# Performance work log

Measured on AMD Instinct MI355X. Metric: run time of the kernel, lower is better.

## Reference

```python
import jax, jax.numpy as jnp
import numpy as np

B, S, D = 4, 2048, 1024
H, HK = 16, 4          # num_heads, num_heads_kv
HD = D // H            # head_dim = 64
G = H // HK            # kv groups = 4


def setup_inputs() -> dict:
    key = jax.random.key(0)
    ks = jax.random.split(key, 7)
    s = 0.02
    return {
        "query": jax.random.normal(ks[0], (B, S, D), jnp.float32),
        "key":   jax.random.normal(ks[1], (B, S, D), jnp.float32),
        "value": jax.random.normal(ks[2], (B, S, D), jnp.float32),
        # weights stored (in, out); equivalent to torch Linear y = x @ W.T
        "Wq": jax.random.normal(ks[3], (D, H * HD), jnp.float32) * s,
        "Wk": jax.random.normal(ks[4], (D, HK * HD), jnp.float32) * s,
        "Wv": jax.random.normal(ks[5], (D, HK * HD), jnp.float32) * s,
        "Wo": jax.random.normal(ks[6], (H * HD, D), jnp.float32) * s,
    }


def reference(query, key, value, Wq, Wk, Wv, Wo):
    b, qlen, _ = query.shape
    kvlen = key.shape[1]
    # projections
    q = (query @ Wq).reshape(b, qlen, H, HD)        # [b,q,H,hd]
    k = (key @ Wk).reshape(b, kvlen, HK, HD)        # [b,s,HK,hd]
    v = (value @ Wv).reshape(b, kvlen, HK, HD)      # [b,s,HK,hd]
    # GQA: q head h attends kv head h//G (repeat_interleave semantics)
    qg = q.reshape(b, qlen, HK, G, HD)              # head = kv*G + group
    scale = 1.0 / jnp.sqrt(jnp.asarray(HD, q.dtype))
    # scores [b,HK,G,q,s] -- broadcast kv heads, no materialized repeat
    scores = jnp.einsum('bqkgd,bskd->bkgqs', qg, k) * scale
    attn = jax.nn.softmax(scores, axis=-1)
    out = jnp.einsum('bkgqs,bskd->bqkgd', attn, v)  # [b,q,HK,G,hd]
    out = out.reshape(b, qlen, H * HD)
    return out @ Wo
```

## Files before the change

kernel.cpp:

```cpp
#include <hip/hip_runtime.h>


typedef unsigned short u16;
typedef unsigned int   u32;
typedef __bf16 bf16x4 __attribute__((ext_vector_type(4)));
typedef __bf16 bf16x8 __attribute__((ext_vector_type(8)));
typedef float  f32x4  __attribute__((ext_vector_type(4)));

#define MFMA(a,b,c) __builtin_amdgcn_mfma_f32_16x16x32_bf16((a),(b),(c),0,0,0)

#define GLDS(g, l) __builtin_amdgcn_global_load_lds(                          \
    (const __attribute__((address_space(1))) void*)(g),                       \
    (__attribute__((address_space(3))) void*)(l), 16, 0, 0)

#if __has_builtin(__builtin_amdgcn_exp2f)
#define EXP2(x) __builtin_amdgcn_exp2f(x)
#else
#define EXP2(x) exp2f(x)
#endif

__device__ __forceinline__ u16 f2bf(float f){
    u32 u = __builtin_bit_cast(u32, f);
    u += 0x7fffu + ((u >> 16) & 1u);
    return (u16)(u >> 16);
}
__device__ __forceinline__ u32 pk2(float a, float b){
#if __has_builtin(__builtin_amdgcn_cvt_pk_bf16_f32)
    auto r = __builtin_amdgcn_cvt_pk_bf16_f32(a, b);
    return __builtin_bit_cast(u32, r);
#else
    return (u32)f2bf(a) | ((u32)f2bf(b) << 16);
#endif
}
__device__ __forceinline__ bf16x8 ldfrag(const u16* p){
    return *(const bf16x8*)p;
}
__device__ __forceinline__ bf16x8 ld2x64(const u16* p){
    bf16x4 lo = *(const bf16x4*)p;
    bf16x4 hi = *(const bf16x4*)(p + 4);
    bf16x8 r;
    r[0]=lo[0]; r[1]=lo[1]; r[2]=lo[2]; r[3]=lo[3];
    r[4]=hi[0]; r[5]=hi[1]; r[6]=hi[2]; r[7]=hi[3];
    return r;
}

__global__ __launch_bounds__(256) void prep(const float* __restrict__ q,
                                            const float* __restrict__ k,
                                            const float* __restrict__ v,
                                            const float* __restrict__ Wq,
                                            const float* __restrict__ Wk,
                                            const float* __restrict__ Wv,
                                            const float* __restrict__ Wo,
                                            u16* Qc, u16* Kc, u16* Vc,
                                            u16* WqT, u16* WkT, u16* WvT, u16* WoT){
    const int tid = threadIdx.x, bid = blockIdx.x;
    if (bid < 2560){
        __shared__ float T[32][33];
        const float* W; u16* WT; int N, i;
        if (bid < 1024)      { W = Wq; WT = WqT; N = 1024; i = bid; }
        else if (bid < 1280) { W = Wk; WT = WkT; N =  256; i = bid - 1024; }
        else if (bid < 1536) { W = Wv; WT = WvT; N =  256; i = bid - 1280; }
        else                 { W = Wo; WT = WoT; N = 1024; i = bid - 1536; }
        int kt = (i & 31) * 32, nt = (i >> 5) * 32;
        int r = tid >> 3, c = tid & 7;
        float4 vv = *(const float4*)(W + (size_t)(kt + r) * N + nt + c * 4);
        T[r][c*4+0] = vv.x; T[r][c*4+1] = vv.y; T[r][c*4+2] = vv.z; T[r][c*4+3] = vv.w;
        __syncthreads();
        u32 lo = pk2(T[c*4+0][r], T[c*4+1][r]);
        u32 hi = pk2(T[c*4+2][r], T[c*4+3][r]);
        *(uint2*)(WT + (size_t)(nt + r) * 1024 + kt + c * 4) = make_uint2(lo, hi);
    } else {
        int i = bid - 2560;
        const float* src = (i < 512) ? q : (i < 1024 ? k : v);
        u16*         dst = (i < 512) ? Qc : (i < 1024 ? Kc : Vc);
        size_t off = (size_t)(i & 511) * 16384;
        const float* s = src + off;
        u16* d = dst + off;
        #pragma unroll
        for (int p = 0; p < 16; ++p){
            int idx = (p * 256 + tid) * 4;
            float4 vv = *(const float4*)(s + idx);
            *(uint2*)(d + idx) = make_uint2(pk2(vv.x, vv.y), pk2(vv.z, vv.w));
        }
    }
}

template<int EPI>
__device__ __forceinline__ void gemm_body(const u16* __restrict__ A,
                                          const u16* __restrict__ Bt,
                                          void* __restrict__ Cp,
                                          int N, int K, int m0, int n0,
                                          u16* As, u16* Bs, float oscale){
    const int tid  = threadIdx.x;
    const int wave = tid >> 6, lane = tid & 63;
    const int quad = lane >> 4, l15 = lane & 15;
    const int wm = wave >> 1, wn = wave & 1;
    const int srow = lane >> 3;
    const int scol = ((lane & 7) ^ srow) * 8;
    const int swz  = l15 & 7;

    f32x4 acc[4][4];
    #pragma unroll
    for (int i = 0; i < 4; ++i)
        #pragma unroll
        for (int j = 0; j < 4; ++j) acc[i][j] = (f32x4){0.f, 0.f, 0.f, 0.f};

    const int nkt = K >> 6;
    for (int kt = 0; kt < nkt; ++kt){
        __syncthreads();
        {
            const u16* ga = A + (size_t)(m0 + wave*32 + srow) * K + kt*64 + scol;
            u16* la = As + (wave*32) * 64;
            #pragma unroll
            for (int p = 0; p < 4; ++p)
                GLDS(ga + (size_t)(p*8) * K, la + p*8*64);
            const u16* gb = Bt + (size_t)(n0 + wave*32 + srow) * K + kt*64 + scol;
            u16* lb = Bs + (wave*32) * 64;
            #pragma unroll
            for (int p = 0; p < 4; ++p)
                GLDS(gb + (size_t)(p*8) * K, lb + p*8*64);
        }
        __syncthreads();
        #pragma unroll
        for (int ks = 0; ks < 2; ++ks){
            bf16x8 af[4], bfr[4];
            #pragma unroll
            for (int mt = 0; mt < 4; ++mt)
                af[mt] = ldfrag(&As[(wm*64 + mt*16 + l15) * 64 +
                                    (((ks*4 + quad) ^ swz) * 8)]);
            #pragma unroll
            for (int nt = 0; nt < 4; ++nt)
                bfr[nt] = ldfrag(&Bs[(wn*64 + nt*16 + l15) * 64 +
                                     (((ks*4 + quad) ^ swz) * 8)]);
            #pragma unroll
            for (int mt = 0; mt < 4; ++mt)
                #pragma unroll
                for (int nt = 0; nt < 4; ++nt){
                    if constexpr (EPI == 1)
                        acc[mt][nt] = MFMA(af[mt], bfr[nt], acc[mt][nt]);
                    else
                        acc[mt][nt] = MFMA(bfr[nt], af[mt], acc[mt][nt]);
                }
        }
    }
    #pragma unroll
    for (int mt = 0; mt < 4; ++mt){
        #pragma unroll
        for (int nt = 0; nt < 4; ++nt){
            if constexpr (EPI == 1){
                int rowb = m0 + wm*64 + mt*16 + quad*4;
                int col  = n0 + wn*64 + nt*16 + l15;
                u16* C = (u16*)Cp;
                int bb = rowb >> 11, s = rowb & 2047;
                u32 lo = pk2(acc[mt][nt][0], acc[mt][nt][1]);
                u32 hi = pk2(acc[mt][nt][2], acc[mt][nt][3]);
                *(uint2*)(C + (size_t)(bb * 256 + col) * 2048 + s) = make_uint2(lo, hi);
            } else {
                int row  = m0 + wm*64 + mt*16 + l15;
                int colb = n0 + wn*64 + nt*16 + quad*4;
                if constexpr (EPI == 0){
                    u16* C = (u16*)Cp;
                    u32 lo = pk2(acc[mt][nt][0]*oscale, acc[mt][nt][1]*oscale);
                    u32 hi = pk2(acc[mt][nt][2]*oscale, acc[mt][nt][3]*oscale);
                    *(uint2*)(C + (size_t)row * N + colb) = make_uint2(lo, hi);
                } else {
                    float* C = (float*)Cp;
                    *(f32x4*)(C + (size_t)row * N + colb) = acc[mt][nt];
                }
            }
        }
    }
}

__global__ __launch_bounds__(256) void gemm_qkv(const u16* Qc, const u16* WqT, u16* Qp,
                                                const u16* Kc, const u16* WkT, u16* Kp,
                                                const u16* Vc, const u16* WvT, u16* Vt,
                                                float qscale){
    __shared__ u16 As[128 * 64];
    __shared__ u16 Bs[128 * 64];
    int bid = blockIdx.x;
    if (bid < 512)
        gemm_body<0>(Qc, WqT, Qp, 1024, 1024, (bid >> 3) * 128, (bid & 7) * 128,
                     As, Bs, qscale);
    else if (bid < 640){
        int i = bid - 512;
        gemm_body<0>(Kc, WkT, Kp, 256, 1024, (i >> 1) * 128, (i & 1) * 128,
                     As, Bs, 1.0f);
    } else {
        int i = bid - 640;
        gemm_body<1>(Vc, WvT, Vt, 256, 1024, (i >> 1) * 128, (i & 1) * 128,
                     As, Bs, 1.0f);
    }
}

__global__ __launch_bounds__(256) void gemm_o(const u16* AO, const u16* WoT,
                                              float* Out){
    __shared__ u16 As[128 * 64];
    __shared__ u16 Bs[128 * 64];
    int bid = blockIdx.x;
    gemm_body<2>(AO, WoT, Out, 1024, 1024, (bid >> 3) * 128, (bid & 7) * 128,
                 As, Bs, 1.0f);
}

__global__ __launch_bounds__(512, 4) void attn_k(const u16* __restrict__ Qp,
                                                 const u16* __restrict__ Kp,
                                                 const u16* __restrict__ Vt,
                                                 u16* __restrict__ AO){
    constexpr int S = 2048, Dm = 1024, NKV = 256, PST = 68;
    __shared__ u16 Kb[2][64 * 64];
    __shared__ u16 Vb[2][64 * 64];
    __shared__ u16 Ps[256 * PST];
    const int tid = threadIdx.x, wave = tid >> 6, lane = tid & 63;
    const int quad = lane >> 4, l15 = lane & 15;
    const int h = blockIdx.y, b = blockIdx.z;
    const int hk = h >> 2, q0 = blockIdx.x * 256;
    u16* pw = Ps + wave * (32 * PST);

    const int srow = lane >> 3;
    const int scol = ((lane & 7) ^ srow) * 8;
    const int swz  = l15 & 7;

    auto issue = [&](int t){
        int j0 = t * 64, bufi = t & 1;
        int r = wave * 8 + srow;
        GLDS(Kp + (size_t)(b * S + j0 + r) * NKV + hk * 64 + scol,
             &Kb[bufi][wave * 8 * 64]);
        GLDS(Vt + (size_t)(b * NKV + hk * 64 + r) * S + j0 + scol,
             &Vb[bufi][wave * 8 * 64]);
    };

    issue(0);
    {
        int c8 = tid & 7, r0 = tid >> 3;
        #pragma unroll
        for (int p = 0; p < 4; ++p){
            int r = r0 + p * 64;
            uint4 v = *(const uint4*)(Qp + (size_t)(b * S + q0 + r) * Dm + h * 64 + c8 * 8);
            *(uint2*)&Ps[r * PST + c8 * 8]     = make_uint2(v.x, v.y);
            *(uint2*)&Ps[r * PST + c8 * 8 + 4] = make_uint2(v.z, v.w);
        }
    }
    __syncthreads();
    bf16x8 qf[2][2];
    #pragma unroll
    for (int mt = 0; mt < 2; ++mt)
        #pragma unroll
        for (int ks = 0; ks < 2; ++ks)
            qf[mt][ks] = ld2x64(&Ps[(wave*32 + mt*16 + l15) * PST + ks*32 + quad*8]);

    const u32 one2 = 0x3F803F80u;
    const bf16x8 ones = __builtin_bit_cast(bf16x8, make_uint4(one2, one2, one2, one2));

    f32x4 O[4][2];
    #pragma unroll
    for (int dt = 0; dt < 4; ++dt)
        #pragma unroll
        for (int mt = 0; mt < 2; ++mt) O[dt][mt] = (f32x4){0.f, 0.f, 0.f, 0.f};
    f32x4 sums[2];
    #pragma unroll
    for (int mt = 0; mt < 2; ++mt) sums[mt] = (f32x4){0.f, 0.f, 0.f, 0.f};

    for (int t = 0; t < 32; ++t){
        __syncthreads();
        if (t < 31) issue(t + 1);
        const u16* Kt = Kb[t & 1];
        const u16* Vs = Vb[t & 1];
        f32x4 sf[2][4];
        #pragma unroll
        for (int mt = 0; mt < 2; ++mt)
            #pragma unroll
            for (int nt = 0; nt < 4; ++nt) sf[mt][nt] = (f32x4){0.f, 0.f, 0.f, 0.f};
        #pragma unroll
        for (int ks = 0; ks < 2; ++ks){
            bf16x8 ak[4];
            #pragma unroll
            for (int nt = 0; nt < 4; ++nt)
                ak[nt] = ldfrag(&Kt[(nt*16 + l15) * 64 + (((ks*4 + quad) ^ swz) * 8)]);
            #pragma unroll
            for (int mt = 0; mt < 2; ++mt)
                #pragma unroll
                for (int nt = 0; nt < 4; ++nt)
                    sf[mt][nt] = MFMA(ak[nt], qf[mt][ks], sf[mt][nt]);
        }
        #pragma unroll
        for (int mt = 0; mt < 2; ++mt)
            #pragma unroll
            for (int nt = 0; nt < 4; ++nt){
                float e0 = EXP2(sf[mt][nt][0]);
                float e1 = EXP2(sf[mt][nt][1]);
                float e2 = EXP2(sf[mt][nt][2]);
                float e3 = EXP2(sf[mt][nt][3]);
                *(uint2*)&pw[(mt*16 + l15) * PST + nt*16 + quad*4] =
                    make_uint2(pk2(e0, e1), pk2(e2, e3));
            }
        __threadfence_block();
        #pragma unroll
        for (int ks = 0; ks < 2; ++ks){
            bf16x8 av[4], bp[2];
            #pragma unroll
            for (int dt = 0; dt < 4; ++dt)
                av[dt] = ldfrag(&Vs[(dt*16 + l15) * 64 + (((ks*4 + quad) ^ swz) * 8)]);
            #pragma unroll
            for (int mt = 0; mt < 2; ++mt)
                bp[mt] = ld2x64(&pw[(mt*16 + l15) * PST + ks*32 + quad*8]);
            #pragma unroll
            for (int mt = 0; mt < 2; ++mt)
                sums[mt] = MFMA(ones, bp[mt], sums[mt]);
            #pragma unroll
            for (int dt = 0; dt < 4; ++dt)
                #pragma unroll
                for (int mt = 0; mt < 2; ++mt)
                    O[dt][mt] = MFMA(av[dt], bp[mt], O[dt][mt]);
        }
    }
    #pragma unroll
    for (int mt = 0; mt < 2; ++mt){
        float inv = 1.0f / sums[mt][0];
        size_t row = (size_t)(b * S + q0 + wave*32 + mt*16 + l15);
        #pragma unroll
        for (int dt = 0; dt < 4; ++dt){
            u32 lo = pk2(O[dt][mt][0] * inv, O[dt][mt][1] * inv);
            u32 hi = pk2(O[dt][mt][2] * inv, O[dt][mt][3] * inv);
            *(uint2*)(AO + row * Dm + h * 64 + dt*16 + quad*4) = make_uint2(lo, hi);
        }
    }
}

extern "C" void kernel_launch(void* const* d_in, const int* in_sizes, int n_in,
                              void* d_out, int out_size, void* d_ws, size_t ws_size,
                              hipStream_t stream){
    const float* q  = (const float*)d_in[0];
    const float* k  = (const float*)d_in[1];
    const float* v  = (const float*)d_in[2];
    const float* Wq = (const float*)d_in[3];
    const float* Wk = (const float*)d_in[4];
    const float* Wv = (const float*)d_in[5];
    const float* Wo = (const float*)d_in[6];
    char* ws = (char*)d_ws;
    const size_t MB = 1u << 20;
    u16* WqT = (u16*)(ws);
    u16* WkT = (u16*)(ws + 2*MB);
    u16* WvT = (u16*)(ws + 2*MB + 512*1024);
    u16* WoT = (u16*)(ws + 3*MB);
    u16* Qc  = (u16*)(ws + 5*MB);
    u16* Kc  = (u16*)(ws + 21*MB);
    u16* Vc  = (u16*)(ws + 37*MB);
    u16* Qp  = (u16*)(ws + 53*MB);
    u16* Kp  = (u16*)(ws + 69*MB);
    u16* Vt  = (u16*)(ws + 73*MB);
    u16* AO  = (u16*)(ws + 5*MB);

    const float cexp = 0.125f * 1.44269504f;

    prep<<<dim3(4096), 256, 0, stream>>>(q, k, v, Wq, Wk, Wv, Wo,
                                         Qc, Kc, Vc, WqT, WkT, WvT, WoT);
    gemm_qkv<<<dim3(768), 256, 0, stream>>>(Qc, WqT, Qp, Kc, WkT, Kp,
                                            Vc, WvT, Vt, cexp);
    attn_k<<<dim3(8, 16, 4), 512, 0, stream>>>(Qp, Kp, Vt, AO);
    gemm_o<<<dim3(512), 256, 0, stream>>>(AO, WoT, (float*)d_out);
}
```

Baseline: 315.0 us.

## Fuse fp32-to-bf16 activation conversion into QKV projection GEMM tile loads

Removes the separate conversion pass that wrote bf16 copies of query, key and value. The QKV GEMM now loads fp32 A tiles directly, converts them to bf16 in registers and stores them into a padded LDS tile (stride 80) instead of using async global-to-LDS loads. This saves a full write and re-read of the converted activations but doubles A-operand bytes per GEMM tile load and replaces the async loads with synchronous register-staged ones.

```diff
diff --git a/kernel.cpp b/kernel.cpp
--- a/kernel.cpp
+++ b/kernel.cpp
@@ -44,53 +44,35 @@
     return r;
 }
 
-__global__ __launch_bounds__(256) void prep(const float* __restrict__ q,
-                                            const float* __restrict__ k,
-                                            const float* __restrict__ v,
-                                            const float* __restrict__ Wq,
+__global__ __launch_bounds__(256) void prep(const float* __restrict__ Wq,
                                             const float* __restrict__ Wk,
                                             const float* __restrict__ Wv,
                                             const float* __restrict__ Wo,
-                                            u16* Qc, u16* Kc, u16* Vc,
                                             u16* WqT, u16* WkT, u16* WvT, u16* WoT){
     const int tid = threadIdx.x, bid = blockIdx.x;
-    if (bid < 2560){
-        __shared__ float T[32][33];
-        const float* W; u16* WT; int N, i;
-        if (bid < 1024)      { W = Wq; WT = WqT; N = 1024; i = bid; }
-        else if (bid < 1280) { W = Wk; WT = WkT; N =  256; i = bid - 1024; }
-        else if (bid < 1536) { W = Wv; WT = WvT; N =  256; i = bid - 1280; }
-        else                 { W = Wo; WT = WoT; N = 1024; i = bid - 1536; }
-        int kt = (i & 31) * 32, nt = (i >> 5) * 32;
-        int r = tid >> 3, c = tid & 7;
-        float4 vv = *(const float4*)(W + (size_t)(kt + r) * N + nt + c * 4);
-        T[r][c*4+0] = vv.x; T[r][c*4+1] = vv.y; T[r][c*4+2] = vv.z; T[r][c*4+3] = vv.w;
-        __syncthreads();
-        u32 lo = pk2(T[c*4+0][r], T[c*4+1][r]);
-        u32 hi = pk2(T[c*4+2][r], T[c*4+3][r]);
-        *(uint2*)(WT + (size_t)(nt + r) * 1024 + kt + c * 4) = make_uint2(lo, hi);
-    } else {
-        int i = bid - 2560;
-        const float* src = (i < 512) ? q : (i < 1024 ? k : v);
-        u16*         dst = (i < 512) ? Qc : (i < 1024 ? Kc : Vc);
-        size_t off = (size_t)(i & 511) * 16384;
-        const float* s = src + off;
-        u16* d = dst + off;
-        #pragma unroll
-        for (int p = 0; p < 16; ++p){
-            int idx = (p * 256 + tid) * 4;
-            float4 vv = *(const float4*)(s + idx);
-            *(uint2*)(d + idx) = make_uint2(pk2(vv.x, vv.y), pk2(vv.z, vv.w));
-        }
-    }
-}
-
-template<int EPI>
-__device__ __forceinline__ void gemm_body(const u16* __restrict__ A,
+    __shared__ float T[32][33];
+    const float* W; u16* WT; int N, i;
+    if (bid < 1024)      { W = Wq; WT = WqT; N = 1024; i = bid; }
+    else if (bid < 1280) { W = Wk; WT = WkT; N =  256; i = bid - 1024; }
+    else if (bid < 1536) { W = Wv; WT = WvT; N =  256; i = bid - 1280; }
+    else                 { W = Wo; WT = WoT; N = 1024; i = bid - 1536; }
+    int kt = (i & 31) * 32, nt = (i >> 5) * 32;
+    int r = tid >> 3, c = tid & 7;
+    float4 vv = *(const float4*)(W + (size_t)(kt + r) * N + nt + c * 4);
+    T[r][c*4+0] = vv.x; T[r][c*4+1] = vv.y; T[r][c*4+2] = vv.z; T[r][c*4+3] = vv.w;
+    __syncthreads();
+    u32 lo = pk2(T[c*4+0][r], T[c*4+1][r]);
+    u32 hi = pk2(T[c*4+2][r], T[c*4+3][r]);
+    *(uint2*)(WT + (size_t)(nt + r) * 1024 + kt + c * 4) = make_uint2(lo, hi);
+}
+
+template<int ATYPE, int EPI>
+__device__ __forceinline__ void gemm_body(const void* __restrict__ Ap,
                                           const u16* __restrict__ Bt,
                                           void* __restrict__ Cp,
                                           int N, int K, int m0, int n0,
                                           u16* As, u16* Bs, float oscale){
+    constexpr int ASTR = (ATYPE == 0) ? 80 : 64;
     const int tid  = threadIdx.x;
     const int wave = tid >> 6, lane = tid & 63;
     const int quad = lane >> 4, l15 = lane & 15;
@@ -108,12 +90,24 @@
     const int nkt = K >> 6;
     for (int kt = 0; kt < nkt; ++kt){
         __syncthreads();
-        {
+        if constexpr (ATYPE == 0){
+            const float* A = (const float*)Ap;
+            int c4 = tid & 15, r0 = tid >> 4;
+            #pragma unroll
+            for (int p = 0; p < 8; ++p){
+                int r = r0 + p * 16;
+                float4 v = *(const float4*)(A + (size_t)(m0 + r) * K + kt * 64 + c4 * 4);
+                *(uint2*)&As[r * 80 + c4 * 4] = make_uint2(pk2(v.x, v.y), pk2(v.z, v.w));
+            }
+        } else {
+            const u16* A = (const u16*)Ap;
             const u16* ga = A + (size_t)(m0 + wave*32 + srow) * K + kt*64 + scol;
             u16* la = As + (wave*32) * 64;
             #pragma unroll
             for (int p = 0; p < 4; ++p)
                 GLDS(ga + (size_t)(p*8) * K, la + p*8*64);
+        }
+        {
             const u16* gb = Bt + (size_t)(n0 + wave*32 + srow) * K + kt*64 + scol;
             u16* lb = Bs + (wave*32) * 64;
             #pragma unroll
@@ -125,9 +119,13 @@
         for (int ks = 0; ks < 2; ++ks){
             bf16x8 af[4], bfr[4];
             #pragma unroll
-            for (int mt = 0; mt < 4; ++mt)
-                af[mt] = ldfrag(&As[(wm*64 + mt*16 + l15) * 64 +
-                                    (((ks*4 + quad) ^ swz) * 8)]);
+            for (int mt = 0; mt < 4; ++mt){
+                if constexpr (ATYPE == 0)
+                    af[mt] = ldfrag(&As[(wm*64 + mt*16 + l15) * 80 + ks*32 + quad*8]);
+                else
+                    af[mt] = ldfrag(&As[(wm*64 + mt*16 + l15) * 64 +
+                                        (((ks*4 + quad) ^ swz) * 8)]);
+            }
             #pragma unroll
             for (int nt = 0; nt < 4; ++nt)
                 bfr[nt] = ldfrag(&Bs[(wn*64 + nt*16 + l15) * 64 +
@@ -172,24 +170,24 @@
     }
 }
 
-__global__ __launch_bounds__(256) void gemm_qkv(const u16* Qc, const u16* WqT, u16* Qp,
-                                                const u16* Kc, const u16* WkT, u16* Kp,
-                                                const u16* Vc, const u16* WvT, u16* Vt,
+__global__ __launch_bounds__(256) void gemm_qkv(const float* q, const u16* WqT, u16* Qp,
+                                                const float* k, const u16* WkT, u16* Kp,
+                                                const float* v, const u16* WvT, u16* Vt,
                                                 float qscale){
-    __shared__ u16 As[128 * 64];
+    __shared__ u16 As[128 * 80];
     __shared__ u16 Bs[128 * 64];
     int bid = blockIdx.x;
     if (bid < 512)
-        gemm_body<0>(Qc, WqT, Qp, 1024, 1024, (bid >> 3) * 128, (bid & 7) * 128,
-                     As, Bs, qscale);
+        gemm_body<0,0>((const void*)q, WqT, (void*)Qp, 1024, 1024,
+                       (bid >> 3) * 128, (bid & 7) * 128, As, Bs, qscale);
     else if (bid < 640){
         int i = bid - 512;
-        gemm_body<0>(Kc, WkT, Kp, 256, 1024, (i >> 1) * 128, (i & 1) * 128,
-                     As, Bs, 1.0f);
+        gemm_body<0,0>((const void*)k, WkT, (void*)Kp, 256, 1024,
+                       (i >> 1) * 128, (i & 1) * 128, As, Bs, 1.0f);
     } else {
         int i = bid - 640;
-        gemm_body<1>(Vc, WvT, Vt, 256, 1024, (i >> 1) * 128, (i & 1) * 128,
-                     As, Bs, 1.0f);
+        gemm_body<0,1>((const void*)v, WvT, (void*)Vt, 256, 1024,
+                       (i >> 1) * 128, (i & 1) * 128, As, Bs, 1.0f);
     }
 }
 
@@ -198,8 +196,8 @@
     __shared__ u16 As[128 * 64];
     __shared__ u16 Bs[128 * 64];
     int bid = blockIdx.x;
-    gemm_body<2>(AO, WoT, Out, 1024, 1024, (bid >> 3) * 128, (bid & 7) * 128,
-                 As, Bs, 1.0f);
+    gemm_body<1,2>((const void*)AO, WoT, (void*)Out, 1024, 1024,
+                   (bid >> 3) * 128, (bid & 7) * 128, As, Bs, 1.0f);
 }
 
 __global__ __launch_bounds__(512, 4) void attn_k(const u16* __restrict__ Qp,
@@ -342,20 +340,16 @@
     u16* WkT = (u16*)(ws + 2*MB);
     u16* WvT = (u16*)(ws + 2*MB + 512*1024);
     u16* WoT = (u16*)(ws + 3*MB);
-    u16* Qc  = (u16*)(ws + 5*MB);
-    u16* Kc  = (u16*)(ws + 21*MB);
-    u16* Vc  = (u16*)(ws + 37*MB);
-    u16* Qp  = (u16*)(ws + 53*MB);
-    u16* Kp  = (u16*)(ws + 69*MB);
-    u16* Vt  = (u16*)(ws + 73*MB);
-    u16* AO  = (u16*)(ws + 5*MB);
+    u16* Qp  = (u16*)(ws + 5*MB);
+    u16* Kp  = (u16*)(ws + 21*MB);
+    u16* Vt  = (u16*)(ws + 25*MB);
+    u16* AO  = (u16*)(ws + 29*MB);
 
     const float cexp = 0.125f * 1.44269504f;
 
-    prep<<<dim3(4096), 256, 0, stream>>>(q, k, v, Wq, Wk, Wv, Wo,
-                                         Qc, Kc, Vc, WqT, WkT, WvT, WoT);
-    gemm_qkv<<<dim3(768), 256, 0, stream>>>(Qc, WqT, Qp, Kc, WkT, Kp,
-                                            Vc, WvT, Vt, cexp);
+    prep<<<dim3(2560), 256, 0, stream>>>(Wq, Wk, Wv, Wo, WqT, WkT, WvT, WoT);
+    gemm_qkv<<<dim3(768), 256, 0, stream>>>(q, WqT, Qp, k, WkT, Kp,
+                                            v, WvT, Vt, cexp);
     attn_k<<<dim3(8, 16, 4), 512, 0, stream>>>(Qp, Kp, Vt, AO);
     gemm_o<<<dim3(512), 256, 0, stream>>>(AO, WoT, (float*)d_out);
 }
```

After: 312.3 us. Within noise of the previous version (-0.9%).
